# Kernel tuning notes

Measured on AMD Instinct MI355X. Metric: run time of the kernel, lower is better.

The kernel has to match this reference:

```python
import jax, jax.numpy as jnp
import numpy as np

N_CELLS = 776
N_ANCHORS = 3
N_CH = 7
CONF_THRESH = 0.8
NO_OBJECT = 0.5


def _iou(pred, label):
    # pred: (2328, 7) anchor boxes in cx,cy,w,h format; label: (7,) gt box
    px, py, pw, ph = pred[:, 0], pred[:, 1], pred[:, 2], pred[:, 3]
    lx, ly, lw, lh = label[0], label[1], label[2], label[3]
    ax = jnp.maximum(px - pw / 2, lx - lw / 2)
    ay = jnp.maximum(py - ph / 2, ly - lh / 2)
    bx = jnp.minimum(px + pw / 2, lx + lw / 2)
    by = jnp.minimum(py + ph / 2, ly + lh / 2)
    intersect = jnp.abs(jnp.maximum(bx - ax, 0.0) * jnp.maximum(by - ay, 0.0))
    area_a = jnp.abs(pw * ph)
    area_b = jnp.abs(lw * lh)
    iou = intersect / (area_a + area_b - intersect)
    return iou.reshape(N_CELLS, N_ANCHORS)


def setup_inputs() -> dict:
    key = jax.random.key(0)
    k1, k2 = jax.random.split(key)
    pred = jax.random.uniform(k1, (N_CELLS * N_ANCHORS, N_CH), dtype=jnp.float32)
    label = jax.random.uniform(k2, (N_CH,), dtype=jnp.float32)
    return {"pred": pred, "label": label}


def reference(pred, label):
    boxes = pred.reshape(N_CELLS, N_ANCHORS, N_CH)          # (776, 3, 7)
    iou = _iou(pred, label)                                  # (776, 3)
    best_idx = jnp.argmax(iou, axis=1)                       # (776,) first-max, matches torch.max
    best = boxes[jnp.arange(N_CELLS), best_idx]              # (776, 7)

    # coord loss (faithful to source: wh term reuses x,y coords, a quirk of the original)
    xy_loss = (label[0] - best[:, 0]) ** 2 + (label[1] - best[:, 1]) ** 2
    wh_loss = (jnp.sqrt(label[0]) - jnp.sqrt(best[:, 0])) ** 2 + \
              (jnp.sqrt(label[1]) - jnp.sqrt(best[:, 1])) ** 2
    coord_loss = xy_loss + wh_loss

    has_obj = best[:, 4] > CONF_THRESH
    class_loss = jnp.where(
        has_obj,
        (label[5] - best[:, 5]) ** 2 + (label[6] - best[:, 6]) ** 2,
        0.0,
    )
    conf_sq = (label[4] - best[:, 4]) ** 2
    conf_loss = jnp.where(has_obj, conf_sq, NO_OBJECT * conf_sq)

    return jnp.sum(coord_loss + class_loss + conf_loss)
```

## Files before the change

kernel.cpp:

```cpp
#include <hip/hip_runtime.h>
#include <hip/hip_bf16.h>

#define N_CELLS 776
#define N_ANCHORS 3
#define N_CH 7
#define CONF_THRESH 0.8f
#define NO_OBJECT 0.5f

__global__ __launch_bounds__(1024) void yolo_loss_kernel(
    const float* __restrict__ pred,
    const float* __restrict__ label,
    float* __restrict__ out)
{
    const int tid = threadIdx.x;

    const float l0 = label[0], l1 = label[1], l2 = label[2], l3 = label[3];
    const float l4 = label[4], l5 = label[5], l6 = label[6];

    float loss = 0.0f;
    if (tid < N_CELLS) {
        const float* row = pred + tid * (N_ANCHORS * N_CH);

        float best_iou = -INFINITY;
        float b[N_CH];
        #pragma unroll
        for (int a = 0; a < N_ANCHORS; ++a) {
            const float* p = row + a * N_CH;
            const float px = p[0], py = p[1], pw = p[2], ph = p[3];
            const float ax = fmaxf(px - pw * 0.5f, l0 - l2 * 0.5f);
            const float ay = fmaxf(py - ph * 0.5f, l1 - l3 * 0.5f);
            const float bx = fminf(px + pw * 0.5f, l0 + l2 * 0.5f);
            const float by = fminf(py + ph * 0.5f, l1 + l3 * 0.5f);
            const float inter = fabsf(fmaxf(bx - ax, 0.0f) * fmaxf(by - ay, 0.0f));
            const float area_a = fabsf(pw * ph);
            const float area_b = fabsf(l2 * l3);
            const float iou = inter / (area_a + area_b - inter);
            if (iou > best_iou) {
                best_iou = iou;
                #pragma unroll
                for (int c = 0; c < N_CH; ++c) b[c] = p[c];
            }
        }

        const float dx = l0 - b[0];
        const float dy = l1 - b[1];
        const float xy_loss = dx * dx + dy * dy;
        const float sw0 = sqrtf(l0) - sqrtf(b[0]);
        const float sw1 = sqrtf(l1) - sqrtf(b[1]);
        const float wh_loss = sw0 * sw0 + sw1 * sw1;
        const float coord_loss = xy_loss + wh_loss;

        const bool has_obj = b[4] > CONF_THRESH;
        const float d5 = l5 - b[5];
        const float d6 = l6 - b[6];
        const float class_loss = has_obj ? (d5 * d5 + d6 * d6) : 0.0f;
        const float d4 = l4 - b[4];
        const float conf_sq = d4 * d4;
        const float conf_loss = has_obj ? conf_sq : NO_OBJECT * conf_sq;

        loss = coord_loss + class_loss + conf_loss;
    }

    #pragma unroll
    for (int off = 32; off > 0; off >>= 1)
        loss += __shfl_down(loss, off, 64);

    __shared__ float smem[16];
    const int wave = tid >> 6;
    if ((tid & 63) == 0) smem[wave] = loss;
    __syncthreads();

    if (tid == 0) {
        float tot = 0.0f;
        #pragma unroll
        for (int w = 0; w < 16; ++w) tot += smem[w];
        out[0] = tot;
    }
}

extern "C" void kernel_launch(void* const* d_in, const int* in_sizes, int n_in,
                              void* d_out, int out_size, void* d_ws, size_t ws_size,
                              hipStream_t stream) {
    const float* pred  = (const float*)d_in[0];
    const float* label = (const float*)d_in[1];
    float* out = (float*)d_out;
    yolo_loss_kernel<<<1, 1024, 0, stream>>>(pred, label, out);
}
```

Measured before the change: 56.60 us.

## Split loss across multiple blocks with LDS-staged coalesced loads and final reduce kernel

Work moves from one 1024-thread block to 13 blocks of 64 threads, one cell per lane. Each block first copies its slice of pred into shared memory with coalesced loads, then reduces across its wave into a per-block partial stored in the workspace. A second single-wave kernel sums the partials. This spreads the loads across several CUs and replaces strided global reads, but adds a second kernel launch and a workspace round trip.

```diff
diff --git a/kernel.cpp b/kernel.cpp
--- a/kernel.cpp
+++ b/kernel.cpp
@@ -7,19 +7,35 @@
 #define CONF_THRESH 0.8f
 #define NO_OBJECT 0.5f
 
-__global__ __launch_bounds__(1024) void yolo_loss_kernel(
+#define CELLS_PER_BLOCK 64
+#define N_BLOCKS ((N_CELLS + CELLS_PER_BLOCK - 1) / CELLS_PER_BLOCK)
+#define DWORDS_PER_BLOCK (CELLS_PER_BLOCK * N_ANCHORS * N_CH)
+
+__global__ __launch_bounds__(64) void yolo_partial_kernel(
     const float* __restrict__ pred,
     const float* __restrict__ label,
-    float* __restrict__ out)
+    float* __restrict__ partials)
 {
-    const int tid = threadIdx.x;
+    const int lane = threadIdx.x;
+    const int blk  = blockIdx.x;
 
     const float l0 = label[0], l1 = label[1], l2 = label[2], l3 = label[3];
     const float l4 = label[4], l5 = label[5], l6 = label[6];
 
+    __shared__ float s[DWORDS_PER_BLOCK];
+    const int gbase = blk * DWORDS_PER_BLOCK;
+    #pragma unroll
+    for (int k = 0; k < 21; ++k) {
+        const int idx = k * 64 + lane;
+        const int g = gbase + idx;
+        if (g < N_CELLS * N_ANCHORS * N_CH) s[idx] = pred[g];
+    }
+    __syncthreads();
+
+    const int cell = blk * CELLS_PER_BLOCK + lane;
     float loss = 0.0f;
-    if (tid < N_CELLS) {
-        const float* row = pred + tid * (N_ANCHORS * N_CH);
+    if (cell < N_CELLS) {
+        const float* row = &s[lane * (N_ANCHORS * N_CH)];
 
         float best_iou = -INFINITY;
         float b[N_CH];
@@ -64,18 +80,19 @@
     #pragma unroll
     for (int off = 32; off > 0; off >>= 1)
         loss += __shfl_down(loss, off, 64);
+    if (lane == 0) partials[blk] = loss;
+}
 
-    __shared__ float smem[16];
-    const int wave = tid >> 6;
-    if ((tid & 63) == 0) smem[wave] = loss;
-    __syncthreads();
-
-    if (tid == 0) {
-        float tot = 0.0f;
-        #pragma unroll
-        for (int w = 0; w < 16; ++w) tot += smem[w];
-        out[0] = tot;
-    }
+__global__ __launch_bounds__(64) void yolo_final_kernel(
+    const float* __restrict__ partials,
+    float* __restrict__ out)
+{
+    const int lane = threadIdx.x;
+    float v = (lane < N_BLOCKS) ? partials[lane] : 0.0f;
+    #pragma unroll
+    for (int off = 32; off > 0; off >>= 1)
+        v += __shfl_down(v, off, 64);
+    if (lane == 0) out[0] = v;
 }
 
 extern "C" void kernel_launch(void* const* d_in, const int* in_sizes, int n_in,
@@ -84,5 +101,8 @@
     const float* pred  = (const float*)d_in[0];
     const float* label = (const float*)d_in[1];
     float* out = (float*)d_out;
-    yolo_loss_kernel<<<1, 1024, 0, stream>>>(pred, label, out);
+    float* partials = (float*)d_ws;
+
+    yolo_partial_kernel<<<N_BLOCKS, CELLS_PER_BLOCK, 0, stream>>>(pred, label, partials);
+    yolo_final_kernel<<<1, 64, 0, stream>>>(partials, out);
 }
```

Result: slower. 64.03 us (+13.1%).
